# Optimization experiments

Hardware: AMD Instinct MI355X
Metric: run time of the kernel (lower is better)

The kernel has to match this reference:

```python
import jax, jax.numpy as jnp
import numpy as np

GROUP = 5  # in-group size implied by `expected_in = indices.shape[1] * 5`


def setup_inputs() -> dict:
    key = jax.random.key(0)
    k1, k2, k3, k4 = jax.random.split(key, 4)
    T, IN, OUT, G, C, K = 64, 4100, 12288, 820, 2, 256
    x = jax.random.normal(k1, (T, IN), dtype=jnp.float32)
    indices = jax.random.randint(k2, (OUT, G, C), 0, K, dtype=jnp.int32)
    codebooks = (jax.random.normal(k3, (C, K, GROUP), dtype=jnp.float32) * 0.05).astype(jnp.float16)
    scales = jax.random.uniform(k4, (OUT,), dtype=jnp.float32, minval=0.5, maxval=1.5)
    return {"x": x, "indices": indices, "codebooks": codebooks, "scales": scales}


def reference(x, indices, codebooks, scales):
    orig_shape = x.shape
    x_flat = x.reshape(-1, orig_shape[-1])
    expected_in = indices.shape[1] * GROUP
    pad = expected_in - x_flat.shape[1]
    if pad > 0:
        x_flat = jnp.pad(x_flat, ((0, 0), (0, pad)))
    # safety scaling (fp16 overflow guard), as in the torch module
    x_max = jnp.maximum(jnp.abs(x_flat).max(), 1.0) * 8.0
    cb_max = jnp.maximum(jnp.abs(codebooks).astype(jnp.float32).max(), 1.0)
    x_safe = (x_flat / x_max).astype(jnp.float16)
    cb_safe = (codebooks.astype(jnp.float32) / cb_max).astype(jnp.float16)
    # additive-codebook dequant: W[o, g] = sum_c cb_safe[c, indices[o,g,c], :]
    C = cb_safe.shape[0]
    gathered = cb_safe[jnp.arange(C)[None, None, :], indices]  # (O, G, C, GROUP) fp16
    W = gathered.sum(axis=2).reshape(indices.shape[0], -1)     # (O, expected_in) fp16
    out = jnp.einsum('ti,oi->to', x_safe, W, preferred_element_type=jnp.float32)
    out = out * x_max.astype(jnp.float32) * cb_max
    out = out * scales[None, :]
    out = jnp.nan_to_num(out, nan=0.0, posinf=0.0, neginf=0.0)
    return out.reshape(*orig_shape[:-1], -1).astype(x.dtype)
```

## Files before the change

### kernel.cpp

```cpp
#include <hip/hip_runtime.h>
#include <hip/hip_fp16.h>
#include <cstdint>

#define T_DIM 64
#define IN_DIM 4100
#define OUT_DIM 12288
#define G_DIM 820
#define KCODE 256
#define GRP 5
#define KP 6560
#define KB32 205
#define CHUNKS 41
#define CH_G 20
#define CH_K 160
#define KSPLIT 4
#define NBLK 192
#define LDS_STRIDE 168

typedef _Float16 f16x8 __attribute__((ext_vector_type(8)));
typedef float f32x4 __attribute__((ext_vector_type(4)));

__device__ float g_pmax[256];
__device__ float g_cbmax;
__device__ float g_xmax;
__device__ __align__(16) _Float16 g_cbq[2 * KCODE * 8];
__device__ __align__(16) _Float16 g_xA[4 * KB32 * 64 * 8];
__device__ __align__(16) float g_part[KSPLIT * T_DIM * OUT_DIM];

__device__ __forceinline__ float block_reduce_max(float m, float* sm) {
    for (int off = 32; off > 0; off >>= 1)
        m = fmaxf(m, __shfl_down(m, off));
    int tid = threadIdx.x;
    if ((tid & 63) == 0) sm[tid >> 6] = m;
    __syncthreads();
    float r = fmaxf(fmaxf(sm[0], sm[1]), fmaxf(sm[2], sm[3]));
    __syncthreads();
    return r;
}

__global__ void __launch_bounds__(256) k1_absmax_cb(const float* __restrict__ x,
                                                    const void* __restrict__ cbraw) {
    __shared__ float sm[4];
    int tid = threadIdx.x, bid = blockIdx.x;
    float m = 0.f;
    for (int i = bid * 256 + tid; i < T_DIM * IN_DIM; i += 256 * 256)
        m = fmaxf(m, fabsf(x[i]));
    float r = block_reduce_max(m, sm);
    if (tid == 0) g_pmax[bid] = r;

    if (bid == 0) {
        unsigned u0 = *(const unsigned*)cbraw;
        bool is_f32 = (((u0 >> 23) & 0xFF) >= 100);
        float mm = 0.f;
        for (int i = tid; i < 2 * KCODE * GRP; i += 256) {
            float v = is_f32 ? ((const float*)cbraw)[i]
                             : (float)((const _Float16*)cbraw)[i];
            mm = fmaxf(mm, fabsf(v));
        }
        float cbm = fmaxf(block_reduce_max(mm, sm), 1.0f);
        if (tid == 0) g_cbmax = cbm;
        for (int e = tid; e < 2 * KCODE; e += 256) {
            f16x8 v = {};
            #pragma unroll
            for (int j = 0; j < GRP; ++j) {
                float w = is_f32 ? ((const float*)cbraw)[e * GRP + j]
                                 : (float)((const _Float16*)cbraw)[e * GRP + j];
                v[j] = (_Float16)(w / cbm);
            }
            *(f16x8*)&g_cbq[e * 8] = v;
        }
    }
}

__global__ void __launch_bounds__(256) k2_quant(const float* __restrict__ x) {
    __shared__ float sm[4];
    int tid = threadIdx.x;
    float xm = fmaxf(block_reduce_max(g_pmax[tid], sm), 1.0f) * 8.0f;
    if (blockIdx.x == 0 && tid == 0) g_xmax = xm;

    int gt = blockIdx.x * 256 + tid;
    int lane = gt & 63;
    int rest = gt >> 6;
    int kb32 = rest % KB32;
    int t16 = rest / KB32;
    int r16 = lane & 15, q = lane >> 4;
    int t = t16 * 16 + r16;
    int g = kb32 * 4 + q;
    const float* xp = x + (size_t)t * IN_DIM + g * GRP;
    f16x8 v = {};
    #pragma unroll
    for (int j = 0; j < GRP; ++j) v[j] = (_Float16)(xp[j] / xm);
    *(f16x8*)&g_xA[(size_t)gt * 8] = v;
}

__global__ void __launch_bounds__(256) k3_gemm(const int* __restrict__ indices) {
    __shared__ alignas(16) _Float16 w_lds[64 * LDS_STRIDE];
    __shared__ f16x8 cb_sh[2 * KCODE];

    int tid = threadIdx.x;
    int nb = blockIdx.x % NBLK;
    int ksp = blockIdx.x / NBLK;
    int n_base = nb * 64;

    for (int e = tid; e < 2 * KCODE; e += 256)
        cb_sh[e] = *(const f16x8*)&g_cbq[e * 8];

    int sro[5], sgl[5];
    #pragma unroll
    for (int j = 0; j < 5; ++j) {
        int s = tid + j * 256;
        sro[j] = s / 20; sgl[j] = s - sro[j] * 20;
    }

    const int c0 = (CHUNKS * ksp) / KSPLIT;
    const int c1 = (CHUNKS * (ksp + 1)) / KSPLIT;
    const int wid = tid >> 6, lane = tid & 63;
    const int q = lane >> 4, r16 = lane & 15;

    f32x4 acc[4] = {};
    int2 idxr[5];
    uint4 ar[5];
    auto prefetch = [&](int c) {
        int g0 = c * CH_G, kb = c * 5;
        #pragma unroll
        for (int j = 0; j < 5; ++j) {
            ar[j] = *(const uint4*)&g_xA[(size_t)((wid * KB32 + kb + j) * 64 + lane) * 8];
            idxr[j] = *(const int2*)&indices[(size_t)(n_base + sro[j]) * (G_DIM * 2)
                                             + (size_t)(g0 + sgl[j]) * 2];
        }
    };

    prefetch(c0);
    __syncthreads();

    for (int c = c0; c < c1; ++c) {
        #pragma unroll
        for (int j = 0; j < 5; ++j) {
            f16x8 w = cb_sh[idxr[j].x] + cb_sh[KCODE + idxr[j].y];
            *(f16x8*)&w_lds[sro[j] * LDS_STRIDE + sgl[j] * 8] = w;
        }
        uint4 acur[5];
        #pragma unroll
        for (int j = 0; j < 5; ++j) acur[j] = ar[j];
        __syncthreads();
        if (c + 1 < c1) prefetch(c + 1);
        #pragma unroll
        for (int kk = 0; kk < 5; ++kk) {
            f16x8 a = *(f16x8*)&acur[kk];
            #pragma unroll
            for (int nt = 0; nt < 4; ++nt) {
                f16x8 b = *(const f16x8*)&w_lds[(nt * 16 + r16) * LDS_STRIDE + kk * 32 + q * 8];
                acc[nt] = __builtin_amdgcn_mfma_f32_16x16x32_f16(a, b, acc[nt], 0, 0, 0);
            }
        }
        __syncthreads();
    }

    float* outp = g_part + (size_t)ksp * (T_DIM * OUT_DIM);
    #pragma unroll
    for (int nt = 0; nt < 4; ++nt) {
        #pragma unroll
        for (int rr = 0; rr < 4; ++rr) {
            int t = wid * 16 + q * 4 + rr;
            int o = n_base + nt * 16 + r16;
            outp[t * OUT_DIM + o] = acc[nt][rr];
        }
    }
}

__global__ void __launch_bounds__(256) k4_final(const float* __restrict__ scales,
                                                float* __restrict__ out) {
    int i4 = blockIdx.x * 256 + threadIdx.x;
    if (i4 >= T_DIM * OUT_DIM / 4) return;
    float s = g_xmax * g_cbmax;
    const f32x4* p = (const f32x4*)g_part;
    const int Q = T_DIM * OUT_DIM / 4;
    f32x4 v0 = p[i4], v1 = p[Q + i4], v2 = p[2 * Q + i4], v3 = p[3 * Q + i4];
    int o4 = i4 % (OUT_DIM / 4);
    f32x4 sc = *(const f32x4*)&scales[o4 * 4];
    f32x4 r;
    #pragma unroll
    for (int j = 0; j < 4; ++j) {
        float v = (v0[j] + v1[j] + v2[j] + v3[j]) * s * sc[j];
        if (!isfinite(v)) v = 0.f;
        r[j] = v;
    }
    ((f32x4*)out)[i4] = r;
}

extern "C" void kernel_launch(void* const* d_in, const int* in_sizes, int n_in,
                              void* d_out, int out_size, void* d_ws, size_t ws_size,
                              hipStream_t stream) {
    const float* x = (const float*)d_in[0];
    const int* indices = (const int*)d_in[1];
    const void* cbraw = (const void*)d_in[2];
    const float* scales = (const float*)d_in[3];
    float* out = (float*)d_out;
    (void)d_ws; (void)ws_size; (void)n_in; (void)in_sizes; (void)out_size;

    k1_absmax_cb<<<256, 256, 0, stream>>>(x, cbraw);
    k2_quant<<<205, 256, 0, stream>>>(x);
    k3_gemm<<<NBLK * KSPLIT, 256, 0, stream>>>(indices);
    k4_final<<<T_DIM * OUT_DIM / 4 / 256, 256, 0, stream>>>(scales, out);
}
```

Baseline: 146.6 us.

## Fuse split-K reduction into GEMM via atomic counter and switch to 32x32 MFMA

Removes the separate finalize kernel. The last split-K block for each column tile, detected with an atomic counter and thread fences, now sums the four partials and applies scaling, the NaN/inf guard and the output write. The GEMM moves from 16x16x32 to 32x32x16 MFMA, with the x layout reshaped into 32-row tiles to match. A-operand loads are now issued per chunk instead of being prefetched across iterations. This saves a launch and one pass over the partials, but exposes global load latency and adds a tail reduction done by only a few blocks.

```diff
diff --git a/kernel.cpp b/kernel.cpp
--- a/kernel.cpp
+++ b/kernel.cpp
@@ -8,23 +8,23 @@
 #define G_DIM 820
 #define KCODE 256
 #define GRP 5
-#define KP 6560
-#define KB32 205
+#define KB16 410
 #define CHUNKS 41
 #define CH_G 20
-#define CH_K 160
 #define KSPLIT 4
 #define NBLK 192
 #define LDS_STRIDE 168
 
 typedef _Float16 f16x8 __attribute__((ext_vector_type(8)));
 typedef float f32x4 __attribute__((ext_vector_type(4)));
+typedef float f32x16 __attribute__((ext_vector_type(16)));
 
 __device__ float g_pmax[256];
 __device__ float g_cbmax;
 __device__ float g_xmax;
+__device__ int   g_cnt[NBLK];
 __device__ __align__(16) _Float16 g_cbq[2 * KCODE * 8];
-__device__ __align__(16) _Float16 g_xA[4 * KB32 * 64 * 8];
+__device__ __align__(16) _Float16 g_xA[2 * KB16 * 64 * 8];
 __device__ __align__(16) float g_part[KSPLIT * T_DIM * OUT_DIM];
 
 __device__ __forceinline__ float block_reduce_max(float m, float* sm) {
@@ -42,6 +42,7 @@
                                                     const void* __restrict__ cbraw) {
     __shared__ float sm[4];
     int tid = threadIdx.x, bid = blockIdx.x;
+    if (tid == 0 && bid < NBLK) g_cnt[bid] = 0;
     float m = 0.f;
     for (int i = bid * 256 + tid; i < T_DIM * IN_DIM; i += 256 * 256)
         m = fmaxf(m, fabsf(x[i]));
@@ -81,21 +82,24 @@
     int gt = blockIdx.x * 256 + tid;
     int lane = gt & 63;
     int rest = gt >> 6;
-    int kb32 = rest % KB32;
-    int t16 = rest / KB32;
-    int r16 = lane & 15, q = lane >> 4;
-    int t = t16 * 16 + r16;
-    int g = kb32 * 4 + q;
+    int kb = rest % KB16;
+    int tt = rest / KB16;
+    int t = tt * 32 + (lane & 31);
+    int g = kb * 2 + (lane >> 5);
     const float* xp = x + (size_t)t * IN_DIM + g * GRP;
+    float inv = 1.0f / xm;
     f16x8 v = {};
     #pragma unroll
-    for (int j = 0; j < GRP; ++j) v[j] = (_Float16)(xp[j] / xm);
+    for (int j = 0; j < GRP; ++j) v[j] = (_Float16)(xp[j] * inv);
     *(f16x8*)&g_xA[(size_t)gt * 8] = v;
 }
 
-__global__ void __launch_bounds__(256) k3_gemm(const int* __restrict__ indices) {
+__global__ void __launch_bounds__(256) k3_gemm(const int* __restrict__ indices,
+                                               const float* __restrict__ scales,
+                                               float* __restrict__ out) {
     __shared__ alignas(16) _Float16 w_lds[64 * LDS_STRIDE];
     __shared__ f16x8 cb_sh[2 * KCODE];
+    __shared__ int s_old;
 
     int tid = threadIdx.x;
     int nb = blockIdx.x % NBLK;
@@ -112,80 +116,81 @@
         sro[j] = s / 20; sgl[j] = s - sro[j] * 20;
     }
 
+    const int wid = tid >> 6, lane = tid & 63;
+    const int trow = wid >> 1, ocol = wid & 1;
+    const int l31 = lane & 31, lh = lane >> 5;
+
     const int c0 = (CHUNKS * ksp) / KSPLIT;
     const int c1 = (CHUNKS * (ksp + 1)) / KSPLIT;
-    const int wid = tid >> 6, lane = tid & 63;
-    const int q = lane >> 4, r16 = lane & 15;
-
-    f32x4 acc[4] = {};
+
+    f32x16 acc = {};
     int2 idxr[5];
-    uint4 ar[5];
-    auto prefetch = [&](int c) {
-        int g0 = c * CH_G, kb = c * 5;
-        #pragma unroll
-        for (int j = 0; j < 5; ++j) {
-            ar[j] = *(const uint4*)&g_xA[(size_t)((wid * KB32 + kb + j) * 64 + lane) * 8];
+    auto pref_idx = [&](int c) {
+        int g0 = c * CH_G;
+        #pragma unroll
+        for (int j = 0; j < 5; ++j)
             idxr[j] = *(const int2*)&indices[(size_t)(n_base + sro[j]) * (G_DIM * 2)
                                              + (size_t)(g0 + sgl[j]) * 2];
-        }
     };
 
-    prefetch(c0);
+    pref_idx(c0);
     __syncthreads();
 
     for (int c = c0; c < c1; ++c) {
+        uint4 ar[10];
+        #pragma unroll
+        for (int s = 0; s < 10; ++s)
+            ar[s] = *(const uint4*)&g_xA[(size_t)(((trow * KB16) + c * 10 + s) * 64 + lane) * 8];
         #pragma unroll
         for (int j = 0; j < 5; ++j) {
             f16x8 w = cb_sh[idxr[j].x] + cb_sh[KCODE + idxr[j].y];
             *(f16x8*)&w_lds[sro[j] * LDS_STRIDE + sgl[j] * 8] = w;
         }
-        uint4 acur[5];
-        #pragma unroll
-        for (int j = 0; j < 5; ++j) acur[j] = ar[j];
         __syncthreads();
-        if (c + 1 < c1) prefetch(c + 1);
-        #pragma unroll
-        for (int kk = 0; kk < 5; ++kk) {
-            f16x8 a = *(f16x8*)&acur[kk];
+        if (c + 1 < c1) pref_idx(c + 1);
+        #pragma unroll
+        for (int s = 0; s < 10; ++s) {
+            f16x8 a = *(f16x8*)&ar[s];
+            f16x8 b = *(const f16x8*)&w_lds[(ocol * 32 + l31) * LDS_STRIDE + s * 16 + lh * 8];
+            acc = __builtin_amdgcn_mfma_f32_32x32x16_f16(a, b, acc, 0, 0, 0);
+        }
+        __syncthreads();
+    }
+
+    float* pp = g_part + (size_t)ksp * (T_DIM * OUT_DIM);
+    int o = n_base + ocol * 32 + l31;
+    #pragma unroll
+    for (int r = 0; r < 16; ++r) {
+        int t = trow * 32 + 4 * lh + (r & 3) + 8 * (r >> 2);
+        pp[t * OUT_DIM + o] = acc[r];
+    }
+
+    __threadfence();
+    if (tid == 0) s_old = atomicAdd(&g_cnt[nb], 1);
+    __syncthreads();
+    if (s_old == KSPLIT - 1) {
+        __threadfence();
+        float s = g_xmax * g_cbmax;
+        const int TO = T_DIM * OUT_DIM;
+        for (int e = tid; e < 64 * 16; e += 256) {
+            int t = e >> 4;
+            int oc = n_base + (e & 15) * 4;
+            const float* pb = g_part + (size_t)t * OUT_DIM + oc;
+            f32x4 v = *(const f32x4*)pb;
+            v += *(const f32x4*)(pb + TO);
+            v += *(const f32x4*)(pb + 2 * TO);
+            v += *(const f32x4*)(pb + 3 * TO);
+            f32x4 sc = *(const f32x4*)&scales[oc];
+            f32x4 r;
             #pragma unroll
-            for (int nt = 0; nt < 4; ++nt) {
-                f16x8 b = *(const f16x8*)&w_lds[(nt * 16 + r16) * LDS_STRIDE + kk * 32 + q * 8];
-                acc[nt] = __builtin_amdgcn_mfma_f32_16x16x32_f16(a, b, acc[nt], 0, 0, 0);
+            for (int j = 0; j < 4; ++j) {
+                float u = v[j] * s * sc[j];
+                if (!isfinite(u)) u = 0.f;
+                r[j] = u;
             }
-        }
-        __syncthreads();
-    }
-
-    float* outp = g_part + (size_t)ksp * (T_DIM * OUT_DIM);
-    #pragma unroll
-    for (int nt = 0; nt < 4; ++nt) {
-        #pragma unroll
-        for (int rr = 0; rr < 4; ++rr) {
-            int t = wid * 16 + q * 4 + rr;
-            int o = n_base + nt * 16 + r16;
-            outp[t * OUT_DIM + o] = acc[nt][rr];
-        }
-    }
-}
-
-__global__ void __launch_bounds__(256) k4_final(const float* __restrict__ scales,
-                                                float* __restrict__ out) {
-    int i4 = blockIdx.x * 256 + threadIdx.x;
-    if (i4 >= T_DIM * OUT_DIM / 4) return;
-    float s = g_xmax * g_cbmax;
-    const f32x4* p = (const f32x4*)g_part;
-    const int Q = T_DIM * OUT_DIM / 4;
-    f32x4 v0 = p[i4], v1 = p[Q + i4], v2 = p[2 * Q + i4], v3 = p[3 * Q + i4];
-    int o4 = i4 % (OUT_DIM / 4);
-    f32x4 sc = *(const f32x4*)&scales[o4 * 4];
-    f32x4 r;
-    #pragma unroll
-    for (int j = 0; j < 4; ++j) {
-        float v = (v0[j] + v1[j] + v2[j] + v3[j]) * s * sc[j];
-        if (!isfinite(v)) v = 0.f;
-        r[j] = v;
-    }
-    ((f32x4*)out)[i4] = r;
+            *(f32x4*)&out[(size_t)t * OUT_DIM + oc] = r;
+        }
+    }
 }
 
 extern "C" void kernel_launch(void* const* d_in, const int* in_sizes, int n_in,
@@ -200,6 +205,5 @@
 
     k1_absmax_cb<<<256, 256, 0, stream>>>(x, cbraw);
     k2_quant<<<205, 256, 0, stream>>>(x);
-    k3_gemm<<<NBLK * KSPLIT, 256, 0, stream>>>(indices);
-    k4_final<<<T_DIM * OUT_DIM / 4 / 256, 256, 0, stream>>>(scales, out);
-}
+    k3_gemm<<<NBLK * KSPLIT, 256, 0, stream>>>(indices, scales, out);
+}
```

Result: slower. 288.3 us (+96.6%).

## Fuse split-K reduction into GEMM via last-block atomic counter

Applied to the files above, without the earlier changes.

Drops the separate finalize kernel. Each GEMM block bumps a per-column-tile atomic counter after writing its partial sums, and the last of the four K-split blocks reduces the partials, applies scales and the nan guard, and writes the output. This saves one launch and a full pass over the partial buffer. It costs threadfences and a serialized tail on the last block of each tile. It also swaps the per-element divide in quantization for a reciprocal multiply, which can change rounding slightly.

```diff
diff --git a/kernel.cpp b/kernel.cpp
--- a/kernel.cpp
+++ b/kernel.cpp
@@ -12,7 +12,6 @@
 #define KB32 205
 #define CHUNKS 41
 #define CH_G 20
-#define CH_K 160
 #define KSPLIT 4
 #define NBLK 192
 #define LDS_STRIDE 168
@@ -23,6 +22,7 @@
 __device__ float g_pmax[256];
 __device__ float g_cbmax;
 __device__ float g_xmax;
+__device__ int   g_cnt[NBLK];
 __device__ __align__(16) _Float16 g_cbq[2 * KCODE * 8];
 __device__ __align__(16) _Float16 g_xA[4 * KB32 * 64 * 8];
 __device__ __align__(16) float g_part[KSPLIT * T_DIM * OUT_DIM];
@@ -42,6 +42,7 @@
                                                     const void* __restrict__ cbraw) {
     __shared__ float sm[4];
     int tid = threadIdx.x, bid = blockIdx.x;
+    if (tid == 0 && bid < NBLK) g_cnt[bid] = 0;
     float m = 0.f;
     for (int i = bid * 256 + tid; i < T_DIM * IN_DIM; i += 256 * 256)
         m = fmaxf(m, fabsf(x[i]));
@@ -87,15 +88,19 @@
     int t = t16 * 16 + r16;
     int g = kb32 * 4 + q;
     const float* xp = x + (size_t)t * IN_DIM + g * GRP;
+    float inv = 1.0f / xm;
     f16x8 v = {};
     #pragma unroll
-    for (int j = 0; j < GRP; ++j) v[j] = (_Float16)(xp[j] / xm);
+    for (int j = 0; j < GRP; ++j) v[j] = (_Float16)(xp[j] * inv);
     *(f16x8*)&g_xA[(size_t)gt * 8] = v;
 }
 
-__global__ void __launch_bounds__(256) k3_gemm(const int* __restrict__ indices) {
+__global__ void __launch_bounds__(256) k3_gemm(const int* __restrict__ indices,
+                                               const float* __restrict__ scales,
+                                               float* __restrict__ out) {
     __shared__ alignas(16) _Float16 w_lds[64 * LDS_STRIDE];
     __shared__ f16x8 cb_sh[2 * KCODE];
+    __shared__ int s_old;
 
     int tid = threadIdx.x;
     int nb = blockIdx.x % NBLK;
@@ -156,36 +161,43 @@
         __syncthreads();
     }
 
-    float* outp = g_part + (size_t)ksp * (T_DIM * OUT_DIM);
+    float* pp = g_part + (size_t)ksp * (T_DIM * OUT_DIM);
     #pragma unroll
     for (int nt = 0; nt < 4; ++nt) {
         #pragma unroll
         for (int rr = 0; rr < 4; ++rr) {
             int t = wid * 16 + q * 4 + rr;
             int o = n_base + nt * 16 + r16;
-            outp[t * OUT_DIM + o] = acc[nt][rr];
-        }
-    }
-}
-
-__global__ void __launch_bounds__(256) k4_final(const float* __restrict__ scales,
-                                                float* __restrict__ out) {
-    int i4 = blockIdx.x * 256 + threadIdx.x;
-    if (i4 >= T_DIM * OUT_DIM / 4) return;
-    float s = g_xmax * g_cbmax;
-    const f32x4* p = (const f32x4*)g_part;
-    const int Q = T_DIM * OUT_DIM / 4;
-    f32x4 v0 = p[i4], v1 = p[Q + i4], v2 = p[2 * Q + i4], v3 = p[3 * Q + i4];
-    int o4 = i4 % (OUT_DIM / 4);
-    f32x4 sc = *(const f32x4*)&scales[o4 * 4];
-    f32x4 r;
-    #pragma unroll
-    for (int j = 0; j < 4; ++j) {
-        float v = (v0[j] + v1[j] + v2[j] + v3[j]) * s * sc[j];
-        if (!isfinite(v)) v = 0.f;
-        r[j] = v;
-    }
-    ((f32x4*)out)[i4] = r;
+            pp[t * OUT_DIM + o] = acc[nt][rr];
+        }
+    }
+
+    __threadfence();
+    if (tid == 0) s_old = atomicAdd(&g_cnt[nb], 1);
+    __syncthreads();
+    if (s_old == KSPLIT - 1) {
+        __threadfence();
+        float s = g_xmax * g_cbmax;
+        const int TO = T_DIM * OUT_DIM;
+        for (int e = tid; e < 64 * 16; e += 256) {
+            int t = e >> 4;
+            int oc = n_base + (e & 15) * 4;
+            const float* pb = g_part + (size_t)t * OUT_DIM + oc;
+            f32x4 v = *(const f32x4*)pb;
+            v += *(const f32x4*)(pb + TO);
+            v += *(const f32x4*)(pb + 2 * TO);
+            v += *(const f32x4*)(pb + 3 * TO);
+            f32x4 sc = *(const f32x4*)&scales[oc];
+            f32x4 r;
+            #pragma unroll
+            for (int j = 0; j < 4; ++j) {
+                float u = v[j] * s * sc[j];
+                if (!isfinite(u)) u = 0.f;
+                r[j] = u;
+            }
+            *(f32x4*)&out[(size_t)t * OUT_DIM + oc] = r;
+        }
+    }
 }
 
 extern "C" void kernel_launch(void* const* d_in, const int* in_sizes, int n_in,
@@ -200,6 +212,5 @@
 
     k1_absmax_cb<<<256, 256, 0, stream>>>(x, cbraw);
     k2_quant<<<205, 256, 0, stream>>>(x);
-    k3_gemm<<<NBLK * KSPLIT, 256, 0, stream>>>(indices);
-    k4_final<<<T_DIM * OUT_DIM / 4 / 256, 256, 0, stream>>>(scales, out);
-}
+    k3_gemm<<<NBLK * KSPLIT, 256, 0, stream>>>(indices, scales, out);
+}
```

Result: slower. 268.6 us (+83.2%).
